# Kernel tuning notes

Hardware: AMD Instinct MI355X
Metric: run time of the kernel (lower is better)

## Reference

```python
import jax, jax.numpy as jnp
import numpy as np

TAU = 0.04
TAU_STU = 0.1
LOCAL_ONLY = 0

B2, N, D = 512, 49, 256   # 2*B samples (two crops), tokens per sample, feat dim
C, K = 128, 128           # num_concepts, queue depth


def _l2norm(x):
    # F.normalize(p=2, dim=-1) with eps=1e-12
    return x / jnp.maximum(jnp.linalg.norm(x, axis=-1, keepdims=True), 1e-12)


def setup_inputs() -> dict:
    key = jax.random.key(0)
    ks = jax.random.split(key, 13)
    return {
        "s_cls_out": jax.random.normal(ks[0], (B2, D), jnp.float32),
        "s_region_out": jax.random.normal(ks[1], (B2, N, D), jnp.float32),
        "s_fea": jax.random.normal(ks[2], (B2, N, D), jnp.float32),
        "t_cls_out": jax.random.normal(ks[3], (B2, D), jnp.float32),
        "t_region_out": jax.random.normal(ks[4], (B2, N, D), jnp.float32),
        "t_fea": jax.random.normal(ks[5], (B2, N, D), jnp.float32),
        "queue_all": jax.random.uniform(ks[6], (C, K, D), jnp.float32),
        "queue_grid_all": jax.random.uniform(ks[7], (C, K, 2 * N, D), jnp.float32),
        "center": jax.random.normal(ks[8], (1, D), jnp.float32),
        "center_grid": jax.random.normal(ks[9], (1, D), jnp.float32),
        "concept_idx": jax.random.randint(ks[10], (B2,), 0, C, jnp.int32),
        "pos_idx": jax.random.randint(ks[11], (B2,), 0, K, jnp.int32),
        "use_queue": jax.random.randint(ks[12], (B2,), 0, 2, jnp.int32) > 0,
    }


def _dequeue(t_cls_out, t_region_out, t_fea, queue_all, queue_grid_all,
             concept_idx, pos_idx, use_queue):
    # vectorized form of the per-sample queue gather with fallback to teacher feats
    n = t_region_out.shape[1]
    q_cls = queue_all[concept_idx, pos_idx]          # [2B, D]
    q_grid = queue_grid_all[concept_idx, pos_idx]    # [2B, 2N, D]
    m1 = use_queue[:, None]
    m2 = use_queue[:, None, None]
    tc = jnp.where(m1, q_cls, t_cls_out)
    tr = jnp.where(m2, q_grid[:, :n], t_region_out)
    tf = jnp.where(m2, q_grid[:, n:], t_fea)
    return tc, tr, tf


def _term(q_cls, s_cls_v, s_reg, s_f, t_reg, t_f):
    # cls-level CE term [B]
    loss = 0.5 * jnp.sum(-q_cls * jax.nn.log_softmax(s_cls_v, axis=-1), axis=-1)
    if LOCAL_ONLY == 1:
        loss = loss * 0.0
    # token-level: match each student token to its most similar teacher token
    sim = jnp.einsum('bnd,bmd->bnm', _l2norm(s_f), _l2norm(t_f))  # [B,N,N]
    ind = jnp.argmax(sim, axis=2)                                  # [B,N]
    t_idx = jnp.take_along_axis(t_reg, ind[:, :, None], axis=1)    # [B,N,D]
    loss_grid = jnp.sum(-t_idx * jax.nn.log_softmax(s_reg, axis=-1), axis=-1).mean(-1)
    loss = loss + (0.0 if LOCAL_ONLY == 2 else 0.5) * loss_grid
    return loss.mean()


def _token_level_esvit(t_cls_out, t_region_out, t_fea, s_cls_out, s_region_out, s_fea,
                       center, center_grid):
    b2, n, d = s_region_out.shape
    b = b2 // 2
    # cat of the two reshaped halves == flat reshape (contiguous halves)
    s_region_f = s_region_out.reshape(b2 * n, d)
    s_fea_f = s_fea.reshape(b2 * n, d)
    t_region_f = t_region_out.reshape(b2 * n, d)
    t_fea_f = t_fea.reshape(b2 * n, d)

    t_cls = jax.lax.stop_gradient(jax.nn.softmax((t_cls_out - center) / TAU, axis=-1))
    t_reg = jax.lax.stop_gradient(jax.nn.softmax((t_region_f - center_grid) / TAU, axis=-1))

    s_cls = s_cls_out / TAU
    s_reg = s_region_f / TAU_STU

    def chunk2(x):
        return x[: x.shape[0] // 2], x[x.shape[0] // 2:]

    t_cls0, t_cls1 = chunk2(t_cls)
    t_reg0, t_reg1 = chunk2(t_reg)
    t_f0, t_f1 = chunk2(t_fea_f)
    s_cls0, s_cls1 = chunk2(s_cls)
    s_reg0, s_reg1 = chunk2(s_reg)
    s_f0, s_f1 = chunk2(s_fea_f)

    rb = lambda x: x.reshape(b, n, d)
    # (iq=0, v=1) and (iq=1, v=0)
    l01 = _term(t_cls0, s_cls1, rb(s_reg1), rb(s_f1), rb(t_reg0), rb(t_f0))
    l10 = _term(t_cls1, s_cls0, rb(s_reg0), rb(s_f0), rb(t_reg1), rb(t_f1))
    total_loss = (l01 + l10) / 2.0
    return total_loss, t_cls_out, t_region_f


def reference(s_cls_out, s_region_out, s_fea, t_cls_out, t_region_out, t_fea,
              queue_all, queue_grid_all, center, center_grid,
              concept_idx, pos_idx, use_queue):
    tc, tr, tf = _dequeue(t_cls_out, t_region_out, t_fea, queue_all, queue_grid_all,
                          concept_idx, pos_idx, use_queue)
    return _token_level_esvit(tc, tr, tf, s_cls_out, s_region_out, s_fea,
                              center, center_grid)
```

## Files before the change

kernel.cpp:

```cpp
#include <hip/hip_runtime.h>
#include <math.h>

namespace {
constexpr int B2v = 512;
constexpr int NR  = 49;
constexpr int NP  = 64;
constexpr int Dv  = 256;
constexpr int KQ  = 128;
constexpr float INV_TAU     = 25.0f;
constexpr float INV_TAU_STU = 10.0f;
}

typedef __attribute__((ext_vector_type(8))) short bf16x8;
typedef __attribute__((ext_vector_type(4))) float f32x4;

__device__ __forceinline__ float wave_max(float v) {
  for (int o = 32; o; o >>= 1) v = fmaxf(v, __shfl_xor(v, o));
  return v;
}
__device__ __forceinline__ float wave_sum(float v) {
  for (int o = 32; o; o >>= 1) v += __shfl_xor(v, o);
  return v;
}
__device__ __forceinline__ short f2bf(float x) {
  unsigned u = __float_as_uint(x);
  u = u + 0x7FFFu + ((u >> 16) & 1u);
  return (short)(u >> 16);
}
__device__ __forceinline__ float bf2f(unsigned short h) {
  return __uint_as_float(((unsigned)h) << 16);
}

__global__ __launch_bounds__(512, 4) void kmain(
    const float* __restrict__ s_cls_out,
    const float* __restrict__ s_region_out,
    const float* __restrict__ s_fea,
    const float* __restrict__ t_cls_out,
    const float* __restrict__ t_region_out,
    const float* __restrict__ t_fea,
    const float* __restrict__ queue_all,
    const float* __restrict__ queue_grid_all,
    const float* __restrict__ center,
    const float* __restrict__ center_grid,
    const int* __restrict__ concept_idx,
    const int* __restrict__ pos_idx,
    const unsigned char* __restrict__ uq,
    float* __restrict__ out_tc,
    float* __restrict__ out_tr,
    float* __restrict__ block_part) {
  __shared__ __align__(16) unsigned short sfb[NP * Dv];
  __shared__ __align__(16) unsigned short tfb[NP * Dv];
  __shared__ float stats[NR * 2];
  __shared__ float rinv[NP];
  __shared__ int ms_lds[NR];
  __shared__ int flags8[8];
  __shared__ float red[8];
  __shared__ float cls_s;

  const int bt = blockIdx.x, bs = bt ^ 256;
  const int tid = threadIdx.x, lane = tid & 63, wave = tid >> 6;

  {
    unsigned w = ((const unsigned*)uq)[tid & 127];
    int a = __any((w & 0xFFFFFF00u) != 0);
    if (lane == 0) flags8[wave] = a;
  }
  __syncthreads();
  int fl = flags8[0] | flags8[1] | flags8[2] | flags8[3] |
           flags8[4] | flags8[5] | flags8[6] | flags8[7];
  const bool isbool = fl != 0;
  const int uqv = isbool ? (int)uq[bt] : ((const int*)uq)[bt];
  const bool use = uqv != 0;
  const size_t qoff = (size_t)concept_idx[bt] * KQ + (size_t)pos_idx[bt];
  const float* qg = queue_grid_all + qoff * (size_t)(2 * NR) * Dv;
  const float* sfsrc = s_fea + (size_t)bs * NR * Dv;
  const float* tfsrc = use ? (qg + (size_t)NR * Dv) : (t_fea + (size_t)bt * NR * Dv);


  for (int q = tid; q < NP * 32; q += 512) {
    const int r = q >> 5, c = q & 31;
    const int dst = r * Dv + ((c ^ (r & 7)) << 3);
    bf16x8 pa = {0, 0, 0, 0, 0, 0, 0, 0};
    bf16x8 pb = {0, 0, 0, 0, 0, 0, 0, 0};
    if (r < NR) {
      const float* ps = sfsrc + (size_t)r * Dv + c * 8;
      const float* pt = tfsrc + (size_t)r * Dv + c * 8;
      float4 s0 = *(const float4*)ps, s1 = *(const float4*)(ps + 4);
      float4 t0 = *(const float4*)pt, t1 = *(const float4*)(pt + 4);
      pa[0] = f2bf(s0.x); pa[1] = f2bf(s0.y); pa[2] = f2bf(s0.z); pa[3] = f2bf(s0.w);
      pa[4] = f2bf(s1.x); pa[5] = f2bf(s1.y); pa[6] = f2bf(s1.z); pa[7] = f2bf(s1.w);
      pb[0] = f2bf(t0.x); pb[1] = f2bf(t0.y); pb[2] = f2bf(t0.z); pb[3] = f2bf(t0.w);
      pb[4] = f2bf(t1.x); pb[5] = f2bf(t1.y); pb[6] = f2bf(t1.z); pb[7] = f2bf(t1.w);
    }
    *(bf16x8*)&sfb[dst] = pa;
    *(bf16x8*)&tfb[dst] = pb;
  }

  float4 yv[7];
  float lsev[7];
#pragma unroll
  for (int j = 0; j < 7; j++) {
    const int n = wave + 8 * j;
    if (n < NR) {
      float4 y4 = *(const float4*)(s_region_out + ((size_t)bs * NR + n) * Dv + lane * 4);
      y4.x *= INV_TAU_STU; y4.y *= INV_TAU_STU;
      y4.z *= INV_TAU_STU; y4.w *= INV_TAU_STU;
      float smax = wave_max(fmaxf(fmaxf(y4.x, y4.y), fmaxf(y4.z, y4.w)));
      float ssum = wave_sum(expf(y4.x - smax) + expf(y4.y - smax) +
                            expf(y4.z - smax) + expf(y4.w - smax));
      yv[j] = y4;
      lsev[j] = smax + logf(ssum);
    }
  }

  const float4 cg4 = *(const float4*)(center_grid + lane * 4);
  for (int r = wave; r < NR; r += 8) {
    const float* src = use ? (qg + (size_t)r * Dv)
                           : (t_region_out + ((size_t)bt * NR + r) * Dv);
    float4 v = *(const float4*)(src + lane * 4);
    float* o = out_tr + ((size_t)bt * NR + r) * Dv + lane * 4;
    o[0] = v.x; o[1] = v.y; o[2] = v.z; o[3] = v.w;
    float x0 = (v.x - cg4.x) * INV_TAU, x1 = (v.y - cg4.y) * INV_TAU;
    float x2 = (v.z - cg4.z) * INV_TAU, x3 = (v.w - cg4.w) * INV_TAU;
    float m = wave_max(fmaxf(fmaxf(x0, x1), fmaxf(x2, x3)));
    float e = wave_sum(expf(x0 - m) + expf(x1 - m) + expf(x2 - m) + expf(x3 - m));
    if (lane == 0) { stats[r * 2] = m; stats[r * 2 + 1] = e; }
  }

  if (wave == 7) {
    const float* tcsrc = use ? (queue_all + qoff * Dv) : (t_cls_out + (size_t)bt * Dv);
    float4 t4 = *(const float4*)(tcsrc + lane * 4);
    float* otc = out_tc + (size_t)bt * Dv + lane * 4;
    otc[0] = t4.x; otc[1] = t4.y; otc[2] = t4.z; otc[3] = t4.w;
    float4 c4 = *(const float4*)(center + lane * 4);
    float x0 = (t4.x - c4.x) * INV_TAU, x1 = (t4.y - c4.y) * INV_TAU;
    float x2 = (t4.z - c4.z) * INV_TAU, x3 = (t4.w - c4.w) * INV_TAU;
    float M = wave_max(fmaxf(fmaxf(x0, x1), fmaxf(x2, x3)));
    float e0 = expf(x0 - M), e1 = expf(x1 - M), e2 = expf(x2 - M), e3 = expf(x3 - M);
    float S = wave_sum(e0 + e1 + e2 + e3);
    float4 s4 = *(const float4*)(s_cls_out + (size_t)bs * Dv + lane * 4);
    float z0 = s4.x * INV_TAU, z1 = s4.y * INV_TAU;
    float z2 = s4.z * INV_TAU, z3 = s4.w * INV_TAU;
    float M2 = wave_max(fmaxf(fmaxf(z0, z1), fmaxf(z2, z3)));
    float S2 = wave_sum(expf(z0 - M2) + expf(z1 - M2) + expf(z2 - M2) + expf(z3 - M2));
    float lse = M2 + logf(S2);
    float cv = 0.5f * wave_sum(e0 * (lse - z0) + e1 * (lse - z1) +
                               e2 * (lse - z2) + e3 * (lse - z3)) / S;
    if (lane == 0) cls_s = cv;
  }
  __syncthreads();

  for (int r = wave; r < NP; r += 8) {
    const int ch = (lane >> 1) ^ (r & 7);
    const unsigned short* p = &tfb[r * Dv + ch * 8 + (lane & 1) * 4];
    float a0 = bf2f(p[0]), a1 = bf2f(p[1]), a2 = bf2f(p[2]), a3 = bf2f(p[3]);
    float ss = wave_sum(a0 * a0 + a1 * a1 + a2 * a2 + a3 * a3);
    if (lane == 0) rinv[r] = 1.0f / fmaxf(sqrtf(ss), 1e-12f);
  }
  __syncthreads();

  if (wave < 4) {
    f32x4 acc[4];
#pragma unroll
    for (int mb = 0; mb < 4; mb++) acc[mb] = (f32x4){0.f, 0.f, 0.f, 0.f};
    const int rsel = lane & 15, g = lane >> 4, rsw = lane & 7;
    const int rowA = (wave << 4) + rsel;
#pragma unroll
    for (int kk = 0; kk < 8; kk++) {
      const int ch = (kk * 4 + g) ^ rsw;
      bf16x8 a = *(const bf16x8*)&sfb[rowA * Dv + (ch << 3)];
#pragma unroll
      for (int mb = 0; mb < 4; mb++) {
        bf16x8 b = *(const bf16x8*)&tfb[((mb << 4) + rsel) * Dv + (ch << 3)];
        acc[mb] = __builtin_amdgcn_mfma_f32_16x16x32_bf16(a, b, acc[mb], 0, 0, 0);
      }
    }
    float bv[4] = {-INFINITY, -INFINITY, -INFINITY, -INFINITY};
    int bm[4] = {999, 999, 999, 999};
#pragma unroll
    for (int mb = 0; mb < 4; mb++) {
      const int m = (mb << 4) + rsel;
      if (m < NR) {
        const float rv = rinv[m];
#pragma unroll
        for (int r = 0; r < 4; r++) {
          float s = acc[mb][r] * rv;
          if (s > bv[r]) { bv[r] = s; bm[r] = m; }
        }
      }
    }
#pragma unroll
    for (int o = 1; o < 16; o <<= 1) {
#pragma unroll
      for (int r = 0; r < 4; r++) {
        float ov = __shfl_xor(bv[r], o);
        int om = __shfl_xor(bm[r], o);
        if (ov > bv[r] || (ov == bv[r] && om < bm[r])) { bv[r] = ov; bm[r] = om; }
      }
    }
    if (rsel == 0) {
#pragma unroll
      for (int r = 0; r < 4; r++) {
        const int n = (wave << 4) + (g << 2) + r;
        if (n < NR) ms_lds[n] = bm[r];
      }
    }
  }
  __syncthreads();

  float4 tv[7];
  int msj[7];
#pragma unroll
  for (int j = 0; j < 7; j++) {
    const int n = wave + 8 * j;
    if (n < NR) {
      const int ms = ms_lds[n];
      msj[j] = ms;
      const float* trow = use ? (qg + (size_t)ms * Dv)
                              : (t_region_out + ((size_t)bt * NR + ms) * Dv);
      tv[j] = *(const float4*)(trow + lane * 4);
    }
  }
  float gacc = 0.f;
#pragma unroll
  for (int j = 0; j < 7; j++) {
    const int n = wave + 8 * j;
    if (n < NR) {
      const int ms = msj[j];
      const float4 v4 = tv[j];
      const float4 y4 = yv[j];
      const float lse = lsev[j];
      float x0 = (v4.x - cg4.x) * INV_TAU, x1 = (v4.y - cg4.y) * INV_TAU;
      float x2 = (v4.z - cg4.z) * INV_TAU, x3 = (v4.w - cg4.w) * INV_TAU;
      float tmax = stats[ms * 2], tsum = stats[ms * 2 + 1];
      float part = wave_sum(expf(x0 - tmax) * (lse - y4.x) +
                            expf(x1 - tmax) * (lse - y4.y) +
                            expf(x2 - tmax) * (lse - y4.z) +
                            expf(x3 - tmax) * (lse - y4.w));
      gacc += part / tsum;
    }
  }
  if (lane == 0) red[wave] = gacc;
  __syncthreads();
  if (tid == 0) {
    float s = red[0] + red[1] + red[2] + red[3] +
              red[4] + red[5] + red[6] + red[7];
    block_part[bt] = cls_s + (0.5f / 49.0f) * s;
  }
}

__global__ __launch_bounds__(256) void k4_final(const float* __restrict__ block_part,
                                                float* __restrict__ out) {
  __shared__ float red[4];
  const int tid = threadIdx.x, lane = tid & 63, wave = tid >> 6;
  float a = block_part[tid] + block_part[tid + 256];
  a = wave_sum(a);
  if (lane == 0) red[wave] = a;
  __syncthreads();
  if (tid == 0)
    out[0] = (red[0] + red[1] + red[2] + red[3]) * (1.0f / 512.0f);
}

extern "C" void kernel_launch(void* const* d_in, const int* in_sizes, int n_in,
                              void* d_out, int out_size, void* d_ws, size_t ws_size,
                              hipStream_t stream) {
  (void)in_sizes; (void)n_in; (void)out_size; (void)ws_size;
  const float* s_cls_out      = (const float*)d_in[0];
  const float* s_region_out   = (const float*)d_in[1];
  const float* s_fea          = (const float*)d_in[2];
  const float* t_cls_out      = (const float*)d_in[3];
  const float* t_region_out   = (const float*)d_in[4];
  const float* t_fea          = (const float*)d_in[5];
  const float* queue_all      = (const float*)d_in[6];
  const float* queue_grid_all = (const float*)d_in[7];
  const float* center         = (const float*)d_in[8];
  const float* center_grid    = (const float*)d_in[9];
  const int* concept_idx      = (const int*)d_in[10];
  const int* pos_idx          = (const int*)d_in[11];
  const unsigned char* use_q  = (const unsigned char*)d_in[12];

  float* out    = (float*)d_out;
  float* out_tc = out + 1;
  float* out_tr = out + 1 + B2v * Dv;

  float* block_part = (float*)d_ws;

  kmain<<<B2v, 512, 0, stream>>>(s_cls_out, s_region_out, s_fea, t_cls_out,
                                 t_region_out, t_fea, queue_all, queue_grid_all,
                                 center, center_grid, concept_idx, pos_idx,
                                 use_q, out_tc, out_tr, block_part);
  k4_final<<<1, 256, 0, stream>>>(block_part, out);
}
```

Measured before the change: 39.48 us.

## Split MFMA similarity across all eight waves and drop extra use_queue barrier

The bf16 MFMA similarity and argmax now run on all eight waves instead of four. Each half of the waves handles two of the four teacher column blocks and writes a per-half best candidate to shared memory, and the two halves are merged when the chosen index is read. The use_queue dtype detection now uses a per-wave ballot instead of a block-wide LDS barrier, and the student feature staging is issued before the dependent teacher-source selection so its loads can start earlier. The cost is extra LDS for the candidate arrays and a second staging loop. Ties between halves go to the lower index, which matches the earlier first-max behaviour.

```diff
diff --git a/kernel.cpp b/kernel.cpp
--- a/kernel.cpp
+++ b/kernel.cpp
@@ -52,48 +52,29 @@
   __shared__ __align__(16) unsigned short tfb[NP * Dv];
   __shared__ float stats[NR * 2];
   __shared__ float rinv[NP];
-  __shared__ int ms_lds[NR];
-  __shared__ int flags8[8];
+  __shared__ float cand_v[2][NP];
+  __shared__ int   cand_m[2][NP];
   __shared__ float red[8];
   __shared__ float cls_s;
 
   const int bt = blockIdx.x, bs = bt ^ 256;
   const int tid = threadIdx.x, lane = tid & 63, wave = tid >> 6;
 
-  {
-    unsigned w = ((const unsigned*)uq)[tid & 127];
-    int a = __any((w & 0xFFFFFF00u) != 0);
-    if (lane == 0) flags8[wave] = a;
-  }
-  __syncthreads();
-  int fl = flags8[0] | flags8[1] | flags8[2] | flags8[3] |
-           flags8[4] | flags8[5] | flags8[6] | flags8[7];
-  const bool isbool = fl != 0;
-  const int uqv = isbool ? (int)uq[bt] : ((const int*)uq)[bt];
-  const bool use = uqv != 0;
-  const size_t qoff = (size_t)concept_idx[bt] * KQ + (size_t)pos_idx[bt];
-  const float* qg = queue_grid_all + qoff * (size_t)(2 * NR) * Dv;
+  const int ci = concept_idx[bt], pi = pos_idx[bt];
+  const uint2 w2 = ((const uint2*)uq)[lane];
   const float* sfsrc = s_fea + (size_t)bs * NR * Dv;
-  const float* tfsrc = use ? (qg + (size_t)NR * Dv) : (t_fea + (size_t)bt * NR * Dv);
-
 
   for (int q = tid; q < NP * 32; q += 512) {
     const int r = q >> 5, c = q & 31;
     const int dst = r * Dv + ((c ^ (r & 7)) << 3);
     bf16x8 pa = {0, 0, 0, 0, 0, 0, 0, 0};
-    bf16x8 pb = {0, 0, 0, 0, 0, 0, 0, 0};
     if (r < NR) {
       const float* ps = sfsrc + (size_t)r * Dv + c * 8;
-      const float* pt = tfsrc + (size_t)r * Dv + c * 8;
       float4 s0 = *(const float4*)ps, s1 = *(const float4*)(ps + 4);
-      float4 t0 = *(const float4*)pt, t1 = *(const float4*)(pt + 4);
       pa[0] = f2bf(s0.x); pa[1] = f2bf(s0.y); pa[2] = f2bf(s0.z); pa[3] = f2bf(s0.w);
       pa[4] = f2bf(s1.x); pa[5] = f2bf(s1.y); pa[6] = f2bf(s1.z); pa[7] = f2bf(s1.w);
-      pb[0] = f2bf(t0.x); pb[1] = f2bf(t0.y); pb[2] = f2bf(t0.z); pb[3] = f2bf(t0.w);
-      pb[4] = f2bf(t1.x); pb[5] = f2bf(t1.y); pb[6] = f2bf(t1.z); pb[7] = f2bf(t1.w);
     }
     *(bf16x8*)&sfb[dst] = pa;
-    *(bf16x8*)&tfb[dst] = pb;
   }
 
   float4 yv[7];
@@ -111,6 +92,26 @@
       yv[j] = y4;
       lsev[j] = smax + logf(ssum);
     }
+  }
+
+  const bool isbool = __any(((w2.x | w2.y) & 0xFFFFFF00u) != 0) != 0;
+  const int uqv = isbool ? (int)uq[bt] : ((const int*)uq)[bt];
+  const bool use = uqv != 0;
+  const size_t qoff = (size_t)ci * KQ + (size_t)pi;
+  const float* qg = queue_grid_all + qoff * (size_t)(2 * NR) * Dv;
+  const float* tfsrc = use ? (qg + (size_t)NR * Dv) : (t_fea + (size_t)bt * NR * Dv);
+
+  for (int q = tid; q < NP * 32; q += 512) {
+    const int r = q >> 5, c = q & 31;
+    const int dst = r * Dv + ((c ^ (r & 7)) << 3);
+    bf16x8 pb = {0, 0, 0, 0, 0, 0, 0, 0};
+    if (r < NR) {
+      const float* pt = tfsrc + (size_t)r * Dv + c * 8;
+      float4 t0 = *(const float4*)pt, t1 = *(const float4*)(pt + 4);
+      pb[0] = f2bf(t0.x); pb[1] = f2bf(t0.y); pb[2] = f2bf(t0.z); pb[3] = f2bf(t0.w);
+      pb[4] = f2bf(t1.x); pb[5] = f2bf(t1.y); pb[6] = f2bf(t1.z); pb[7] = f2bf(t1.w);
+    }
+    *(bf16x8*)&tfb[dst] = pb;
   }
 
   const float4 cg4 = *(const float4*)(center_grid + lane * 4);
@@ -159,32 +160,34 @@
   }
   __syncthreads();
 
-  if (wave < 4) {
-    f32x4 acc[4];
-#pragma unroll
-    for (int mb = 0; mb < 4; mb++) acc[mb] = (f32x4){0.f, 0.f, 0.f, 0.f};
+  {
+    const int half = wave >> 2, wr = wave & 3;
+    f32x4 acc[2];
+    acc[0] = (f32x4){0.f, 0.f, 0.f, 0.f};
+    acc[1] = (f32x4){0.f, 0.f, 0.f, 0.f};
     const int rsel = lane & 15, g = lane >> 4, rsw = lane & 7;
-    const int rowA = (wave << 4) + rsel;
+    const int rowA = (wr << 4) + rsel;
 #pragma unroll
     for (int kk = 0; kk < 8; kk++) {
       const int ch = (kk * 4 + g) ^ rsw;
       bf16x8 a = *(const bf16x8*)&sfb[rowA * Dv + (ch << 3)];
 #pragma unroll
-      for (int mb = 0; mb < 4; mb++) {
+      for (int mh = 0; mh < 2; mh++) {
+        const int mb = half * 2 + mh;
         bf16x8 b = *(const bf16x8*)&tfb[((mb << 4) + rsel) * Dv + (ch << 3)];
-        acc[mb] = __builtin_amdgcn_mfma_f32_16x16x32_bf16(a, b, acc[mb], 0, 0, 0);
+        acc[mh] = __builtin_amdgcn_mfma_f32_16x16x32_bf16(a, b, acc[mh], 0, 0, 0);
       }
     }
     float bv[4] = {-INFINITY, -INFINITY, -INFINITY, -INFINITY};
     int bm[4] = {999, 999, 999, 999};
 #pragma unroll
-    for (int mb = 0; mb < 4; mb++) {
-      const int m = (mb << 4) + rsel;
+    for (int mh = 0; mh < 2; mh++) {
+      const int m = ((half * 2 + mh) << 4) + rsel;
       if (m < NR) {
         const float rv = rinv[m];
 #pragma unroll
         for (int r = 0; r < 4; r++) {
-          float s = acc[mb][r] * rv;
+          float s = acc[mh][r] * rv;
           if (s > bv[r]) { bv[r] = s; bm[r] = m; }
         }
       }
@@ -201,8 +204,9 @@
     if (rsel == 0) {
 #pragma unroll
       for (int r = 0; r < 4; r++) {
-        const int n = (wave << 4) + (g << 2) + r;
-        if (n < NR) ms_lds[n] = bm[r];
+        const int n = (wr << 4) + (g << 2) + r;
+        cand_v[half][n] = bv[r];
+        cand_m[half][n] = bm[r];
       }
     }
   }
@@ -214,7 +218,7 @@
   for (int j = 0; j < 7; j++) {
     const int n = wave + 8 * j;
     if (n < NR) {
-      const int ms = ms_lds[n];
+      const int ms = (cand_v[1][n] > cand_v[0][n]) ? cand_m[1][n] : cand_m[0][n];
       msj[j] = ms;
       const float* trow = use ? (qg + (size_t)ms * Dv)
                               : (t_region_out + ((size_t)bt * NR + ms) * Dv);
```

After: 38.28 us. -3.0%, faster.
